# Kernel tuning notes

Hardware: AMD Instinct MI355X
Metric: run time of the kernel (lower is better)

The kernel has to match this reference:

```python
import jax, jax.numpy as jnp
import numpy as np
from math import sqrt

D_MODEL = 1024
N_HEADS = 16
D_V = D_MODEL // N_HEADS
D_FF = 4 * D_MODEL
EPS = 1e-5


def setup_inputs() -> dict:
    key = jax.random.key(0)
    ks = jax.random.split(key, 12)
    N, L = 2, 2048
    s = 0.02
    return {
        'queries': jax.random.normal(ks[0], (N, L, D_MODEL), jnp.float32),
        'keys': jax.random.normal(ks[1], (N, L, D_MODEL), jnp.float32),
        'values': jax.random.normal(ks[2], (N, L, D_MODEL), jnp.float32),
        'mask': jnp.ones((N, 1, 1, L), jnp.int32),
        'fc_w': jax.random.normal(ks[3], (D_MODEL, D_MODEL), jnp.float32) * s,
        'fc_b': jnp.zeros((D_MODEL,), jnp.float32),
        'ln1_g': jnp.ones((D_MODEL,), jnp.float32),
        'ln1_b': jnp.zeros((D_MODEL,), jnp.float32),
        'ff_w1': jax.random.normal(ks[4], (D_MODEL, D_FF), jnp.float32) * s,
        'ff_b1': jnp.zeros((D_FF,), jnp.float32),
        'ff_w2': jax.random.normal(ks[5], (D_FF, D_MODEL), jnp.float32) * s,
        'ff_b2': jnp.zeros((D_MODEL,), jnp.float32),
        'ln2_g': jnp.ones((D_MODEL,), jnp.float32),
        'ln2_b': jnp.zeros((D_MODEL,), jnp.float32),
    }


def layer_norm(x, g, b):
    mu = jnp.mean(x, axis=-1, keepdims=True)
    var = jnp.mean(jnp.square(x - mu), axis=-1, keepdims=True)
    return (x - mu) * jax.lax.rsqrt(var + EPS) * g + b


def reference(queries, keys, values, mask, fc_w, fc_b, ln1_g, ln1_b,
              ff_w1, ff_b1, ff_w2, ff_b2, ln2_g, ln2_b):
    N, Lq, _ = queries.shape
    Lk = keys.shape[1]
    # NOTE: the original module never applies its Q/K/V linear layers; raw
    # inputs are reshaped directly into heads.
    q = queries.reshape(N, Lq, N_HEADS, D_V).transpose(0, 2, 1, 3)  # nhqd
    k = keys.reshape(N, Lk, N_HEADS, D_V)                           # nlhd
    v = values.reshape(N, Lk, N_HEADS, D_V)                         # nlhd
    energy = jnp.einsum('nhqd,nlhd->nhql', q, k)
    energy = jnp.where(mask == 0, -jnp.inf, energy)
    # original scales by sqrt(d_model), not sqrt(d_v)
    attn = jax.nn.softmax(energy / sqrt(D_MODEL), axis=-1)
    out = jnp.einsum('nhql,nlhd->nqhd', attn, v).reshape(N, Lq, D_MODEL)
    attention = out @ fc_w + fc_b
    x1 = layer_norm(attention + queries, ln1_g, ln1_b)
    fc = jax.nn.relu(x1 @ ff_w1 + ff_b1) @ ff_w2 + ff_b2
    x2 = layer_norm(fc + x1, ln2_g, ln2_b)
    return x2
```

## Files before the change

### kernel.cpp

```cpp
#include <hip/hip_runtime.h>
#include <stdint.h>

typedef unsigned short u16;
typedef __bf16 bf16x8 __attribute__((ext_vector_type(8), may_alias));
typedef float f32x4 __attribute__((ext_vector_type(4), may_alias));

typedef void __attribute__((address_space(1))) as1_void;
typedef void __attribute__((address_space(3))) as3_void;

#define MFMA16 __builtin_amdgcn_mfma_f32_16x16x32_bf16

__device__ __forceinline__ void async_copy16(const void* g, void* l) {
    __builtin_amdgcn_global_load_lds((as1_void*)g, (as3_void*)l, 16, 0, 0);
}

__device__ __forceinline__ u16 f2bf(float f) {
    union { float f; unsigned u; } c; c.f = f;
    unsigned u = c.u;
    u += 0x7fffu + ((u >> 16) & 1u);
    return (u16)(u >> 16);
}

__global__ __launch_bounds__(256) void cast_f32_bf16(
    const float* __restrict__ in, u16* __restrict__ out, int n4, float scale) {
    int i = blockIdx.x * 256 + threadIdx.x;
    if (i < n4) {
        f32x4 v = *(const f32x4*)&in[(size_t)i * 4];
        ushort4 o;
        o.x = f2bf(v[0] * scale); o.y = f2bf(v[1] * scale);
        o.z = f2bf(v[2] * scale); o.w = f2bf(v[3] * scale);
        *(ushort4*)&out[(size_t)i * 4] = o;
    }
}

__global__ __launch_bounds__(256) void transpose_cast(
    const float* __restrict__ in, u16* __restrict__ out, int R, int C) {
    __shared__ float tile[64][65];
    const float* inb = in + (size_t)blockIdx.z * R * C;
    u16* outb = out + (size_t)blockIdx.z * R * C;
    int t = threadIdx.x;
    int c0 = blockIdx.x * 64, r0 = blockIdx.y * 64;
    int tr = t >> 4, tc = (t & 15) * 4;
#pragma unroll
    for (int p = 0; p < 4; ++p) {
        int r = tr + p * 16;
        f32x4 v = *(const f32x4*)&inb[(size_t)(r0 + r) * C + c0 + tc];
        tile[r][tc] = v[0]; tile[r][tc + 1] = v[1];
        tile[r][tc + 2] = v[2]; tile[r][tc + 3] = v[3];
    }
    __syncthreads();
    int wc = t >> 4, wr = (t & 15) * 4;
#pragma unroll
    for (int p = 0; p < 4; ++p) {
        int cl = wc + p * 16;
        ushort4 o;
        o.x = f2bf(tile[wr + 0][cl]); o.y = f2bf(tile[wr + 1][cl]);
        o.z = f2bf(tile[wr + 2][cl]); o.w = f2bf(tile[wr + 3][cl]);
        *(ushort4*)&outb[(size_t)(c0 + cl) * R + r0 + wr] = o;
    }
}

__global__ __launch_bounds__(256) void flash_attn(
    const u16* __restrict__ Q, const u16* __restrict__ Kb,
    const u16* __restrict__ VT, const int* __restrict__ mask,
    u16* __restrict__ O) {
    __shared__ u16 kls[2][8192];
    __shared__ u16 vls[8192];
    __shared__ u16 pls[8][2048];

    const int bid = blockIdx.x;
    const int qt = bid & 15;
    const int h = (bid >> 4) & 15;
    const int n = bid >> 8;
    const int t = threadIdx.x;
    const int w = t >> 6, lane = t & 63;
    const int m16 = lane & 15, quad = lane >> 4;

    const size_t qrowA = (size_t)(n * 2048 + qt * 128 + w * 16 + m16);
    const size_t qrowB = qrowA + 64;
    bf16x8 qfA0 = *(const bf16x8*)&Q[qrowA * 1024 + h * 64 + quad * 8];
    bf16x8 qfA1 = *(const bf16x8*)&Q[qrowA * 1024 + h * 64 + 32 + quad * 8];
    bf16x8 qfB0 = *(const bf16x8*)&Q[qrowB * 1024 + h * 64 + quad * 8];
    bf16x8 qfB1 = *(const bf16x8*)&Q[qrowB * 1024 + h * 64 + 32 + quad * 8];

    const int* maskn = mask + n * 2048;
    int allones;
    {
        int ok = 1;
#pragma unroll
        for (int i = 0; i < 8; ++i) {
            int4 mv = *(const int4*)&maskn[lane * 32 + i * 4];
            ok &= (mv.x != 0) & (mv.y != 0) & (mv.z != 0) & (mv.w != 0);
        }
        allones = __all(ok);
    }

    f32x4 otA[4] = {}, otB[4] = {};
    f32x4 sumA = {}, sumB = {};

    const u16* Kbase = Kb + (size_t)(n * 2048) * 1024 + h * 64;
    const u16* Vbase = VT + (size_t)(n * 1024 + h * 64) * 2048;
    u16* pwA = &pls[w * 2][0];
    u16* pwB = &pls[w * 2 + 1][0];

#pragma unroll
    for (int i = 0; i < 4; ++i) {
        int e = w * 4 + i;
        async_copy16(&Kbase[(size_t)((e >> 1) * 16 + m16) * 1024 + (e & 1) * 32 + quad * 8],
                     &kls[0][e * 512]);
    }
    __syncthreads();

    for (int kt = 0; kt < 16; ++kt) {
        const u16* kcur = kls[kt & 1];
        if (kt + 1 < 16) {
            u16* knext = kls[(kt + 1) & 1];
#pragma unroll
            for (int i = 0; i < 4; ++i) {
                int e = w * 4 + i;
                async_copy16(&Kbase[(size_t)((kt + 1) * 128 + (e >> 1) * 16 + m16) * 1024 +
                                    (e & 1) * 32 + quad * 8], &knext[e * 512]);
            }
        }
#pragma unroll
        for (int i = 0; i < 4; ++i) {
            int e = w * 4 + i;
            async_copy16(&Vbase[(size_t)((e >> 2) * 16 + m16) * 2048 + kt * 128 +
                                (e & 3) * 32 + quad * 8], &vls[e * 512]);
        }

        f32x4 sA[8] = {}, sB[8] = {};
#pragma unroll
        for (int ct = 0; ct < 8; ++ct) {
            bf16x8 a0 = *(const bf16x8*)&kcur[(ct * 2 + 0) * 512 + lane * 8];
            bf16x8 a1 = *(const bf16x8*)&kcur[(ct * 2 + 1) * 512 + lane * 8];
            sA[ct] = MFMA16(a0, qfA0, sA[ct], 0, 0, 0);
            sA[ct] = MFMA16(a1, qfA1, sA[ct], 0, 0, 0);
            sB[ct] = MFMA16(a0, qfB0, sB[ct], 0, 0, 0);
            sB[ct] = MFMA16(a1, qfB1, sB[ct], 0, 0, 0);
        }

        if (allones) {
#pragma unroll
            for (int ct = 0; ct < 8; ++ct) {
                int c = ct * 2 + (quad >> 1);
                int off = m16 * 128 + (((c ^ m16) & 15) << 3) + (quad & 1) * 4;
                {
                    float p0 = __builtin_amdgcn_exp2f(sA[ct][0]);
                    float p1 = __builtin_amdgcn_exp2f(sA[ct][1]);
                    float p2 = __builtin_amdgcn_exp2f(sA[ct][2]);
                    float p3 = __builtin_amdgcn_exp2f(sA[ct][3]);
                    sumA[0] += p0; sumA[1] += p1; sumA[2] += p2; sumA[3] += p3;
                    unsigned lo = __builtin_amdgcn_perm(__float_as_uint(p1), __float_as_uint(p0), 0x07060302);
                    unsigned hi = __builtin_amdgcn_perm(__float_as_uint(p3), __float_as_uint(p2), 0x07060302);
                    *(uint2*)&pwA[off] = make_uint2(lo, hi);
                }
                {
                    float p0 = __builtin_amdgcn_exp2f(sB[ct][0]);
                    float p1 = __builtin_amdgcn_exp2f(sB[ct][1]);
                    float p2 = __builtin_amdgcn_exp2f(sB[ct][2]);
                    float p3 = __builtin_amdgcn_exp2f(sB[ct][3]);
                    sumB[0] += p0; sumB[1] += p1; sumB[2] += p2; sumB[3] += p3;
                    unsigned lo = __builtin_amdgcn_perm(__float_as_uint(p1), __float_as_uint(p0), 0x07060302);
                    unsigned hi = __builtin_amdgcn_perm(__float_as_uint(p3), __float_as_uint(p2), 0x07060302);
                    *(uint2*)&pwB[off] = make_uint2(lo, hi);
                }
            }
        } else {
#pragma unroll
            for (int ct = 0; ct < 8; ++ct) {
                const int4 mv = *(const int4*)&maskn[kt * 128 + ct * 16 + quad * 4];
                int c = ct * 2 + (quad >> 1);
                int off = m16 * 128 + (((c ^ m16) & 15) << 3) + (quad & 1) * 4;
                {
                    float p0 = __builtin_amdgcn_exp2f(sA[ct][0]) * (mv.x ? 1.f : 0.f);
                    float p1 = __builtin_amdgcn_exp2f(sA[ct][1]) * (mv.y ? 1.f : 0.f);
                    float p2 = __builtin_amdgcn_exp2f(sA[ct][2]) * (mv.z ? 1.f : 0.f);
                    float p3 = __builtin_amdgcn_exp2f(sA[ct][3]) * (mv.w ? 1.f : 0.f);
                    sumA[0] += p0; sumA[1] += p1; sumA[2] += p2; sumA[3] += p3;
                    unsigned lo = __builtin_amdgcn_perm(__float_as_uint(p1), __float_as_uint(p0), 0x07060302);
                    unsigned hi = __builtin_amdgcn_perm(__float_as_uint(p3), __float_as_uint(p2), 0x07060302);
                    *(uint2*)&pwA[off] = make_uint2(lo, hi);
                }
                {
                    float p0 = __builtin_amdgcn_exp2f(sB[ct][0]) * (mv.x ? 1.f : 0.f);
                    float p1 = __builtin_amdgcn_exp2f(sB[ct][1]) * (mv.y ? 1.f : 0.f);
                    float p2 = __builtin_amdgcn_exp2f(sB[ct][2]) * (mv.z ? 1.f : 0.f);
                    float p3 = __builtin_amdgcn_exp2f(sB[ct][3]) * (mv.w ? 1.f : 0.f);
                    sumB[0] += p0; sumB[1] += p1; sumB[2] += p2; sumB[3] += p3;
                    unsigned lo = __builtin_amdgcn_perm(__float_as_uint(p1), __float_as_uint(p0), 0x07060302);
                    unsigned hi = __builtin_amdgcn_perm(__float_as_uint(p3), __float_as_uint(p2), 0x07060302);
                    *(uint2*)&pwB[off] = make_uint2(lo, hi);
                }
            }
        }

        __syncthreads();

        bf16x8 pfA[4], pfB[4];
#pragma unroll
        for (int kc2 = 0; kc2 < 4; ++kc2) {
            int off = m16 * 128 + ((((kc2 * 4 + quad) ^ m16) & 15) << 3);
            pfA[kc2] = *(const bf16x8*)&pwA[off];
            pfB[kc2] = *(const bf16x8*)&pwB[off];
        }
#pragma unroll
        for (int kc2 = 0; kc2 < 4; ++kc2) {
#pragma unroll
            for (int dt = 0; dt < 4; ++dt) {
                bf16x8 vf = *(const bf16x8*)&vls[(dt * 4 + kc2) * 512 + lane * 8];
                otA[dt] = MFMA16(vf, pfA[kc2], otA[dt], 0, 0, 0);
                otB[dt] = MFMA16(vf, pfB[kc2], otB[dt], 0, 0, 0);
            }
        }
        __syncthreads();
    }

    float lA = (sumA[0] + sumA[1]) + (sumA[2] + sumA[3]);
    float lB = (sumB[0] + sumB[1]) + (sumB[2] + sumB[3]);
    lA += __shfl_xor(lA, 16); lA += __shfl_xor(lA, 32);
    lB += __shfl_xor(lB, 16); lB += __shfl_xor(lB, 32);
    float invA = 1.f / fmaxf(lA, 1e-30f);
    float invB = 1.f / fmaxf(lB, 1e-30f);

    const size_t obA = qrowA * 1024 + h * 64;
    const size_t obB = qrowB * 1024 + h * 64;
#pragma unroll
    for (int dt = 0; dt < 4; ++dt) {
        unsigned lo = (unsigned)f2bf(otA[dt][0] * invA) | ((unsigned)f2bf(otA[dt][1] * invA) << 16);
        unsigned hi = (unsigned)f2bf(otA[dt][2] * invA) | ((unsigned)f2bf(otA[dt][3] * invA) << 16);
        *(uint2*)&O[obA + dt * 16 + quad * 4] = make_uint2(lo, hi);
        lo = (unsigned)f2bf(otB[dt][0] * invB) | ((unsigned)f2bf(otB[dt][1] * invB) << 16);
        hi = (unsigned)f2bf(otB[dt][2] * invB) | ((unsigned)f2bf(otB[dt][3] * invB) << 16);
        *(uint2*)&O[obB + dt * 16 + quad * 4] = make_uint2(lo, hi);
    }
}

template <int BM, int BN, int RELU, int OUTBF, int SPLITK>
__global__ __launch_bounds__(256) void gemm_bt(
    const u16* __restrict__ A, const u16* __restrict__ Bt,
    const float* __restrict__ bias, void* __restrict__ Cout,
    void* __restrict__ Cout1, int M, int N, int K) {
    constexpr int MI = BM / 32;
    constexpr int NJ = BN / 32;
    __shared__ u16 sm[2][(BM + BN) * 64];
    const int lane = threadIdx.x & 63;
    const int w = threadIdx.x >> 6;
    const int m16 = lane & 15, quad = lane >> 4;
    const int nBn = N / BN;
    int bid = blockIdx.x;
    int slice = 0;
    if (SPLITK > 1) {
        const int nblk = (M / BM) * nBn;
        slice = bid / nblk;
        bid = bid - slice * nblk;
    }
    const int bm = bid / nBn, bn = bid % nBn;
    const int r2 = w >> 1, c2 = w & 1;
    const int Ks = K / SPLITK;
    const int kOff = slice * Ks;

    const u16* Abase = A + (size_t)(bm * BM + m16) * K + quad * 8;
    const u16* Bbase = Bt + (size_t)(bn * BN + m16) * K + quad * 8;

    auto stage = [&](int buf, int k0) {
        u16* smA = &sm[buf][0];
        u16* smB = smA + BM * 64;
#pragma unroll
        for (int i = 0; i < MI; ++i) {
            int e = w * MI + i;
            async_copy16(&Abase[(size_t)((e >> 1) * 16) * K + k0 + (e & 1) * 32], &smA[e * 512]);
        }
#pragma unroll
        for (int i = 0; i < NJ; ++i) {
            int e = w * NJ + i;
            async_copy16(&Bbase[(size_t)((e >> 1) * 16) * K + k0 + (e & 1) * 32], &smB[e * 512]);
        }
    };

    f32x4 acc[MI][NJ] = {};
    const int nK = Ks >> 6;
    stage(0, kOff);
    __syncthreads();
    for (int kt = 0; kt < nK; ++kt) {
        if (kt + 1 < nK) stage((kt + 1) & 1, kOff + ((kt + 1) << 6));
        const u16* smA = &sm[kt & 1][0];
        const u16* smB = smA + BM * 64;
#pragma unroll
        for (int kc = 0; kc < 2; ++kc) {
            bf16x8 a[MI], b[NJ];
#pragma unroll
            for (int i = 0; i < MI; ++i)
                a[i] = *(const bf16x8*)&smA[((r2 * MI + i) * 2 + kc) * 512 + lane * 8];
#pragma unroll
            for (int j = 0; j < NJ; ++j)
                b[j] = *(const bf16x8*)&smB[((c2 * NJ + j) * 2 + kc) * 512 + lane * 8];
#pragma unroll
            for (int i = 0; i < MI; ++i)
#pragma unroll
                for (int j = 0; j < NJ; ++j)
                    acc[i][j] = MFMA16(a[i], b[j], acc[i][j], 0, 0, 0);
        }
        __syncthreads();
    }
    float bv[NJ];
#pragma unroll
    for (int j = 0; j < NJ; ++j)
        bv[j] = (SPLITK == 1 || slice == 0)
                    ? bias[bn * BN + c2 * (BN / 2) + j * 16 + m16] : 0.f;
    void* Csel = (SPLITK > 1 && slice != 0) ? Cout1 : Cout;
#pragma unroll
    for (int i = 0; i < MI; ++i) {
        int row0 = bm * BM + r2 * (BM / 2) + i * 16 + quad * 4;
#pragma unroll
        for (int j = 0; j < NJ; ++j) {
            int col = bn * BN + c2 * (BN / 2) + j * 16 + m16;
#pragma unroll
            for (int r = 0; r < 4; ++r) {
                float v = acc[i][j][r] + bv[j];
                if (RELU) v = fmaxf(v, 0.f);
                size_t idx = (size_t)(row0 + r) * N + col;
                if (OUTBF) ((u16*)Csel)[idx] = f2bf(v);
                else ((float*)Csel)[idx] = v;
            }
        }
    }
}

__global__ __launch_bounds__(256) void ln_residual(
    const float* __restrict__ x, const float* __restrict__ x2,
    const float* __restrict__ res,
    const float* __restrict__ g, const float* __restrict__ b,
    float* __restrict__ out_f32, u16* __restrict__ out_bf16) {
    __shared__ float smr[8];
    int row = blockIdx.x;
    int t = threadIdx.x;
    f32x4 xv = *(const f32x4*)&x[(size_t)row * 1024 + t * 4];
    f32x4 rv = *(const f32x4*)&res[(size_t)row * 1024 + t * 4];
    xv += rv;
    if (x2) {
        f32x4 pv = *(const f32x4*)&x2[(size_t)row * 1024 + t * 4];
        xv += pv;
    }
    float s = xv[0] + xv[1] + xv[2] + xv[3];
    float ss = xv[0] * xv[0] + xv[1] * xv[1] + xv[2] * xv[2] + xv[3] * xv[3];
#pragma unroll
    for (int d = 1; d < 64; d <<= 1) {
        s += __shfl_xor(s, d);
        ss += __shfl_xor(ss, d);
    }
    int w = t >> 6, lane = t & 63;
    if (lane == 0) { smr[w] = s; smr[4 + w] = ss; }
    __syncthreads();
    s = smr[0] + smr[1] + smr[2] + smr[3];
    ss = smr[4] + smr[5] + smr[6] + smr[7];
    float mu = s * (1.f / 1024.f);
    float var = ss * (1.f / 1024.f) - mu * mu;
    float rs = rsqrtf(var + 1e-5f);
    f32x4 gv = *(const f32x4*)&g[t * 4];
    f32x4 bv = *(const f32x4*)&b[t * 4];
    f32x4 y;
#pragma unroll
    for (int i = 0; i < 4; ++i) y[i] = (xv[i] - mu) * rs * gv[i] + bv[i];
    *(f32x4*)&out_f32[(size_t)row * 1024 + t * 4] = y;
    if (out_bf16) {
        ushort4 o;
        o.x = f2bf(y[0]); o.y = f2bf(y[1]); o.z = f2bf(y[2]); o.w = f2bf(y[3]);
        *(ushort4*)&out_bf16[(size_t)row * 1024 + t * 4] = o;
    }
}

extern "C" void kernel_launch(void* const* d_in, const int* in_sizes, int n_in,
                              void* d_out, int out_size, void* d_ws, size_t ws_size,
                              hipStream_t stream) {
    const float* q = (const float*)d_in[0];
    const float* k = (const float*)d_in[1];
    const float* v = (const float*)d_in[2];
    const int* mask = (const int*)d_in[3];
    const float* fc_b = (const float*)d_in[5];
    const float* ln1_g = (const float*)d_in[6];
    const float* ln1_b = (const float*)d_in[7];
    const float* ff_b1 = (const float*)d_in[9];
    const float* ff_b2 = (const float*)d_in[11];
    const float* ln2_g = (const float*)d_in[12];
    const float* ln2_b = (const float*)d_in[13];
    const float* fc_w = (const float*)d_in[4];
    const float* ff_w1 = (const float*)d_in[8];
    const float* ff_w2 = (const float*)d_in[10];

    char* ws = (char*)d_ws;
    const size_t MB = 1024 * 1024;
    u16* qbf = (u16*)(ws + 0);
    u16* kbf = (u16*)(ws + 8 * MB);
    u16* vT  = (u16*)(ws + 16 * MB);
    u16* ao  = (u16*)(ws + 24 * MB);
    u16* hbuf = (u16*)(ws + 0);
    u16* fcwT = (u16*)(ws + 32 * MB);
    u16* w1T  = (u16*)(ws + 34 * MB);
    u16* w2T  = (u16*)(ws + 42 * MB);
    float* attn_raw = (float*)(ws + 50 * MB);
    float* fc_raw   = (float*)(ws + 50 * MB);
    float* x1   = (float*)(ws + 66 * MB);
    u16* x1bf   = (u16*)(ws + 82 * MB);
    float* attn_rawB = (float*)(ws + 0);
    float* fcB = (float*)(ws + 90 * MB);
    const bool big = ws_size >= 106 * MB;

    const float k2 = 0.03125f * 1.44269504088896340736f;

    cast_f32_bf16<<<4096, 256, 0, stream>>>(q, qbf, 1048576, k2);
    cast_f32_bf16<<<4096, 256, 0, stream>>>(k, kbf, 1048576, 1.0f);
    transpose_cast<<<dim3(16, 32, 2), 256, 0, stream>>>(v, vT, 2048, 1024);
    transpose_cast<<<dim3(16, 16, 1), 256, 0, stream>>>(fc_w, fcwT, 1024, 1024);
    transpose_cast<<<dim3(64, 16, 1), 256, 0, stream>>>(ff_w1, w1T, 1024, 4096);
    transpose_cast<<<dim3(16, 64, 1), 256, 0, stream>>>(ff_w2, w2T, 4096, 1024);

    flash_attn<<<512, 256, 0, stream>>>(qbf, kbf, vT, mask, ao);

    gemm_bt<128, 128, 0, 0, 2><<<32 * 8 * 2, 256, 0, stream>>>(
        ao, fcwT, fc_b, attn_raw, attn_rawB, 4096, 1024, 1024);
    ln_residual<<<4096, 256, 0, stream>>>(attn_raw, attn_rawB, q, ln1_g, ln1_b, x1, x1bf);

    gemm_bt<128, 128, 1, 1, 1><<<32 * 32, 256, 0, stream>>>(
        x1bf, w1T, ff_b1, hbuf, nullptr, 4096, 4096, 1024);

    if (big) {
        gemm_bt<128, 128, 0, 0, 2><<<32 * 8 * 2, 256, 0, stream>>>(
            hbuf, w2T, ff_b2, fc_raw, fcB, 4096, 1024, 4096);
        ln_residual<<<4096, 256, 0, stream>>>(fc_raw, fcB, x1, ln2_g, ln2_b,
                                              (float*)d_out, (u16*)nullptr);
    } else {
        gemm_bt<64, 128, 0, 0, 1><<<64 * 8, 256, 0, stream>>>(
            hbuf, w2T, ff_b2, fc_raw, nullptr, 4096, 1024, 4096);
        ln_residual<<<4096, 256, 0, stream>>>(fc_raw, nullptr, x1, ln2_g, ln2_b,
                                              (float*)d_out, (u16*)nullptr);
    }
}
```

Before: 385.9 us.

## Add 256x256 eight-phase pipelined GEMM for FFN layers with 4-way split-K

```diff
diff --git a/kernel.cpp b/kernel.cpp
--- a/kernel.cpp
+++ b/kernel.cpp
@@ -9,6 +9,15 @@
 typedef void __attribute__((address_space(3))) as3_void;
 
 #define MFMA16 __builtin_amdgcn_mfma_f32_16x16x32_bf16
+
+#define SBAR()                                \
+    do {                                      \
+        asm volatile("" ::: "memory");        \
+        __builtin_amdgcn_s_barrier();         \
+        asm volatile("" ::: "memory");        \
+    } while (0)
+#define WAITV(n) asm volatile("s_waitcnt vmcnt(" #n ")" ::: "memory")
+#define WAITL0() asm volatile("s_waitcnt lgkmcnt(0)" ::: "memory")
 
 __device__ __forceinline__ void async_copy16(const void* g, void* l) {
     __builtin_amdgcn_global_load_lds((as1_void*)g, (as3_void*)l, 16, 0, 0);
@@ -320,6 +329,162 @@
                 float v = acc[i][j][r] + bv[j];
                 if (RELU) v = fmaxf(v, 0.f);
                 size_t idx = (size_t)(row0 + r) * N + col;
+                if (OUTBF) ((u16*)Cout)[idx] = f2bf(v);
+                else ((float*)Csel)[idx] = v;
+                (void)Csel;
+            }
+        }
+    }
+}
+
+template <int RELU, int OUTBF, int SPLITK>
+__global__ __launch_bounds__(512, 2) void gemm_8ph(
+    const u16* __restrict__ A, const u16* __restrict__ Bt,
+    const float* __restrict__ bias,
+    void* __restrict__ C0, void* __restrict__ C1,
+    void* __restrict__ C2a, void* __restrict__ C2b, void* __restrict__ C3,
+    int M, int N, int K) {
+    __shared__ u16 sm[2][2][16384];
+    const int t = threadIdx.x;
+    const int w = t >> 6, lane = t & 63;
+    const int m16 = lane & 15, quad = lane >> 4;
+    const int wm = w >> 2, wn = w & 3;
+    const int nBn = N >> 8;
+    int bid = blockIdx.x, slice = 0;
+    if (SPLITK > 1) {
+        const int nblk = (M >> 8) * nBn;
+        slice = bid / nblk;
+        bid -= slice * nblk;
+    }
+    const int bm = bid / nBn, bn = bid % nBn;
+    const int Ks = K / SPLITK;
+    const int nK = Ks >> 6, nIter = nK >> 1;
+    const u16* Abase = A + (size_t)(bm * 256 + m16) * K + slice * Ks + quad * 8;
+    const u16* Bbase = Bt + (size_t)(bn * 256 + m16) * K + slice * Ks + quad * 8;
+
+    auto stage_ht = [&](int h) {
+        if (h < 4 * nK) {
+            const int kt = h >> 2, q = h & 3;
+            const u16* base = (q < 2) ? Abase : Bbase;
+            u16* lds = &sm[kt & 1][q >> 1][0];
+            const int h0 = (q & 1) * 16;
+#pragma unroll
+            for (int i = 0; i < 2; ++i) {
+                const int e = h0 + i * 8 + w;
+                async_copy16(&base[(size_t)((e >> 1) * 16) * K + (size_t)kt * 64 + (e & 1) * 32],
+                             &lds[e * 512]);
+            }
+        }
+    };
+    auto ldsA = [&](int buf, int mf, int kc) {
+        return *(const bf16x8*)&sm[buf][0][((wm * 8 + mf) * 2 + kc) * 512 + lane * 8];
+    };
+    auto ldsB = [&](int buf, int nf, int kc) {
+        return *(const bf16x8*)&sm[buf][1][((wn * 4 + nf) * 2 + kc) * 512 + lane * 8];
+    };
+
+    f32x4 acc[8][4] = {};
+    bf16x8 a0[4][2], a1[4][2], b[4][2];
+
+#define QUAD(Ar, BO, MO, NO)                                                    \
+    do {                                                                        \
+        __builtin_amdgcn_s_setprio(1);                                          \
+        _Pragma("unroll") for (int mi = 0; mi < 4; ++mi)                        \
+            _Pragma("unroll") for (int nj = 0; nj < 2; ++nj)                    \
+                _Pragma("unroll") for (int kc = 0; kc < 2; ++kc)                \
+                    acc[(MO) + mi][(NO) + nj] =                                 \
+                        MFMA16(Ar[mi][kc], b[(BO) + nj][kc],                    \
+                               acc[(MO) + mi][(NO) + nj], 0, 0, 0);             \
+        __builtin_amdgcn_s_setprio(0);                                          \
+    } while (0)
+
+    stage_ht(0); stage_ht(1); stage_ht(2); stage_ht(3);
+    WAITV(4);
+    stage_ht(4); stage_ht(5); stage_ht(6);
+    WAITV(6);
+    SBAR();
+
+    for (int it = 0; it < nIter; ++it) {
+        const int hb = it * 8;
+#pragma unroll
+        for (int mf = 0; mf < 4; ++mf) { a0[mf][0] = ldsA(0, mf, 0); a0[mf][1] = ldsA(0, mf, 1); }
+#pragma unroll
+        for (int nf = 0; nf < 2; ++nf) { b[nf][0] = ldsB(0, nf, 0); b[nf][1] = ldsB(0, nf, 1); }
+        stage_ht(hb + 7);
+        SBAR(); WAITL0();
+        QUAD(a0, 0, 0, 0);
+        SBAR();
+#pragma unroll
+        for (int mf = 0; mf < 4; ++mf) { a1[mf][0] = ldsA(0, mf + 4, 0); a1[mf][1] = ldsA(0, mf + 4, 1); }
+#pragma unroll
+        for (int nf = 0; nf < 2; ++nf) { b[2 + nf][0] = ldsB(0, 2 + nf, 0); b[2 + nf][1] = ldsB(0, 2 + nf, 1); }
+        stage_ht(hb + 8);
+        SBAR(); WAITL0();
+        QUAD(a0, 2, 0, 2);
+        SBAR();
+        stage_ht(hb + 9);
+        SBAR(); WAITL0();
+        QUAD(a1, 2, 4, 2);
+        SBAR();
+        stage_ht(hb + 10);
+        if (it == nIter - 1) { WAITV(0); } else { WAITV(6); }
+        SBAR(); WAITL0();
+        QUAD(a1, 0, 4, 0);
+        SBAR();
+#pragma unroll
+        for (int mf = 0; mf < 4; ++mf) { a0[mf][0] = ldsA(1, mf, 0); a0[mf][1] = ldsA(1, mf, 1); }
+#pragma unroll
+        for (int nf = 0; nf < 2; ++nf) { b[nf][0] = ldsB(1, nf, 0); b[nf][1] = ldsB(1, nf, 1); }
+        stage_ht(hb + 11);
+        SBAR(); WAITL0();
+        QUAD(a0, 0, 0, 0);
+        SBAR();
+#pragma unroll
+        for (int mf = 0; mf < 4; ++mf) { a1[mf][0] = ldsA(1, mf + 4, 0); a1[mf][1] = ldsA(1, mf + 4, 1); }
+#pragma unroll
+        for (int nf = 0; nf < 2; ++nf) { b[2 + nf][0] = ldsB(1, 2 + nf, 0); b[2 + nf][1] = ldsB(1, 2 + nf, 1); }
+        stage_ht(hb + 12);
+        SBAR(); WAITL0();
+        QUAD(a0, 2, 0, 2);
+        SBAR();
+        stage_ht(hb + 13);
+        SBAR(); WAITL0();
+        QUAD(a1, 2, 4, 2);
+        SBAR();
+        stage_ht(hb + 14);
+        if (it + 1 < nIter) { WAITV(6); } else { WAITV(0); }
+        SBAR(); WAITL0();
+        QUAD(a1, 0, 4, 0);
+        SBAR();
+    }
+#undef QUAD
+
+    float bv[4];
+#pragma unroll
+    for (int nf = 0; nf < 4; ++nf)
+        bv[nf] = (SPLITK == 1 || slice == 0) ? bias[bn * 256 + wn * 64 + nf * 16 + m16] : 0.f;
+    void* Csel = C0;
+    int rowAdj = 0;
+    if (SPLITK > 1) {
+        if (slice == 1) Csel = C1;
+        else if (slice == 3) Csel = C3;
+        else if (slice == 2) {
+            const int half = M >> 9;
+            if (bm < half) Csel = C2a;
+            else { Csel = C2b; rowAdj = M >> 1; }
+        }
+    }
+    const int colb = bn * 256 + wn * 64 + m16;
+#pragma unroll
+    for (int mf = 0; mf < 8; ++mf) {
+        const int row0 = bm * 256 + wm * 128 + mf * 16 + quad * 4 - rowAdj;
+#pragma unroll
+        for (int nf = 0; nf < 4; ++nf) {
+#pragma unroll
+            for (int r = 0; r < 4; ++r) {
+                float v = acc[mf][nf][r] + bv[nf];
+                if (RELU) v = fmaxf(v, 0.f);
+                size_t idx = (size_t)(row0 + r) * N + colb + nf * 16;
                 if (OUTBF) ((u16*)Csel)[idx] = f2bf(v);
                 else ((float*)Csel)[idx] = v;
             }
@@ -328,20 +493,24 @@
 }
 
 __global__ __launch_bounds__(256) void ln_residual(
-    const float* __restrict__ x, const float* __restrict__ x2,
+    const float* x, const float* x2,
+    const float* x3a, const float* x3b, const float* x4,
     const float* __restrict__ res,
     const float* __restrict__ g, const float* __restrict__ b,
-    float* __restrict__ out_f32, u16* __restrict__ out_bf16) {
+    float* out_f32, u16* __restrict__ out_bf16) {
     __shared__ float smr[8];
     int row = blockIdx.x;
     int t = threadIdx.x;
     f32x4 xv = *(const f32x4*)&x[(size_t)row * 1024 + t * 4];
     f32x4 rv = *(const f32x4*)&res[(size_t)row * 1024 + t * 4];
     xv += rv;
-    if (x2) {
-        f32x4 pv = *(const f32x4*)&x2[(size_t)row * 1024 + t * 4];
-        xv += pv;
-    }
+    if (x2) xv += *(const f32x4*)&x2[(size_t)row * 1024 + t * 4];
+    if (x3a) {
+        const float* p = (row < 2048) ? x3a + (size_t)row * 1024
+                                      : x3b + (size_t)(row - 2048) * 1024;
+        xv += *(const f32x4*)&p[t * 4];
+    }
+    if (x4) xv += *(const f32x4*)&x4[(size_t)row * 1024 + t * 4];
     float s = xv[0] + xv[1] + xv[2] + xv[3];
     float ss = xv[0] * xv[0] + xv[1] * xv[1] + xv[2] * xv[2] + xv[3] * xv[3];
 #pragma unroll
@@ -403,7 +572,9 @@
     float* x1   = (float*)(ws + 66 * MB);
     u16* x1bf   = (u16*)(ws + 82 * MB);
     float* attn_rawB = (float*)(ws + 0);
-    float* fcB = (float*)(ws + 90 * MB);
+    float* fcB  = (float*)(ws + 90 * MB);
+    float* fcC_lo = (float*)(ws + 32 * MB);
+    float* fcC_hi = (float*)(ws + 82 * MB);
     const bool big = ws_size >= 106 * MB;
 
     const float k2 = 0.03125f * 1.44269504088896340736f;
@@ -419,20 +590,22 @@
 
     gemm_bt<128, 128, 0, 0, 2><<<32 * 8 * 2, 256, 0, stream>>>(
         ao, fcwT, fc_b, attn_raw, attn_rawB, 4096, 1024, 1024);
-    ln_residual<<<4096, 256, 0, stream>>>(attn_raw, attn_rawB, q, ln1_g, ln1_b, x1, x1bf);
-
-    gemm_bt<128, 128, 1, 1, 1><<<32 * 32, 256, 0, stream>>>(
-        x1bf, w1T, ff_b1, hbuf, nullptr, 4096, 4096, 1024);
+    ln_residual<<<4096, 256, 0, stream>>>(attn_raw, attn_rawB, nullptr, nullptr, nullptr,
+                                          q, ln1_g, ln1_b, x1, x1bf);
+
+    gemm_8ph<1, 1, 1><<<256, 512, 0, stream>>>(
+        x1bf, w1T, ff_b1, hbuf, nullptr, nullptr, nullptr, nullptr, 4096, 4096, 1024);
 
     if (big) {
-        gemm_bt<128, 128, 0, 0, 2><<<32 * 8 * 2, 256, 0, stream>>>(
-            hbuf, w2T, ff_b2, fc_raw, fcB, 4096, 1024, 4096);
-        ln_residual<<<4096, 256, 0, stream>>>(fc_raw, fcB, x1, ln2_g, ln2_b,
-                                              (float*)d_out, (u16*)nullptr);
+        gemm_8ph<0, 0, 4><<<256, 512, 0, stream>>>(
+            hbuf, w2T, ff_b2, fc_raw, fcB, fcC_lo, fcC_hi, (float*)d_out,
+            4096, 1024, 4096);
+        ln_residual<<<4096, 256, 0, stream>>>(fc_raw, fcB, fcC_lo, fcC_hi, (float*)d_out,
+                                              x1, ln2_g, ln2_b, (float*)d_out, (u16*)nullptr);
     } else {
         gemm_bt<64, 128, 0, 0, 1><<<64 * 8, 256, 0, stream>>>(
             hbuf, w2T, ff_b2, fc_raw, nullptr, 4096, 1024, 4096);
-        ln_residual<<<4096, 256, 0, stream>>>(fc_raw, nullptr, x1, ln2_g, ln2_b,
-                                              (float*)d_out, (u16*)nullptr);
-    }
-}
+        ln_residual<<<4096, 256, 0, stream>>>(fc_raw, nullptr, nullptr, nullptr, nullptr,
+                                              x1, ln2_g, ln2_b, (float*)d_out, (u16*)nullptr);
+    }
+}
```

After: 381.1 us. No clear change (-1.2%).
